# Optimization experiments

Measured on AMD Instinct MI355X. Metric: run time of the kernel, lower is better.

The kernel has to match this reference:

```python
import jax, jax.numpy as jnp
import numpy as np

NUM_HEADS = 32
NUM_KV_HEADS = 8
HEAD_DIM = 128
ROPE_THETA = 10000.0


def rotate_half(x):
    x1, x2 = jnp.split(x, 2, axis=-1)
    return jnp.concatenate((-x2, x1), axis=-1)


def setup_inputs() -> dict:
    key = jax.random.key(0)
    ks = jax.random.split(key, 5)
    B, S, H = 1, 2048, 4096
    KV = NUM_KV_HEADS * HEAD_DIM
    return {
        "hidden_states": jax.random.normal(ks[0], (B, S, H), dtype=jnp.float32),
        "position_ids": jnp.arange(S, dtype=jnp.int64 if jax.config.jax_enable_x64 else jnp.int32)[None, :].repeat(B, axis=0),
        "Wq": jax.random.normal(ks[1], (H, H), dtype=jnp.float32) * 0.02,
        "Wk": jax.random.normal(ks[2], (KV, H), dtype=jnp.float32) * 0.02,
        "Wv": jax.random.normal(ks[3], (KV, H), dtype=jnp.float32) * 0.02,
        "Wo": jax.random.normal(ks[4], (H, H), dtype=jnp.float32) * 0.02,
    }


def reference(hidden_states, position_ids, Wq, Wk, Wv, Wo):
    B, S, H = hidden_states.shape
    nh, nkv, hd = NUM_HEADS, NUM_KV_HEADS, HEAD_DIM
    n_rep = nh // nkv

    # QKV projections (torch Linear: y = x @ W^T)
    q = jnp.einsum('bsh,oh->bso', hidden_states, Wq).reshape(B, S, nh, hd).transpose(0, 2, 1, 3)
    k = jnp.einsum('bsh,oh->bso', hidden_states, Wk).reshape(B, S, nkv, hd).transpose(0, 2, 1, 3)
    v = jnp.einsum('bsh,oh->bso', hidden_states, Wv).reshape(B, S, nkv, hd).transpose(0, 2, 1, 3)

    # RoPE: cos/sin [B, 1, S, hd]
    inv_freq = 1.0 / (ROPE_THETA ** (jnp.arange(0, hd, 2, dtype=jnp.float32) / hd))
    freqs = position_ids.astype(jnp.float32)[..., None] * inv_freq  # [B, S, hd/2]
    emb = jnp.concatenate((freqs, freqs), axis=-1)                  # [B, S, hd]
    cos = jnp.cos(emb)[:, None, :, :]
    sin = jnp.sin(emb)[:, None, :, :]
    q = q * cos + rotate_half(q) * sin
    k = k * cos + rotate_half(k) * sin

    # GQA repeat_kv: [B, nkv, S, hd] -> [B, nh, S, hd]
    k = jnp.repeat(k, n_rep, axis=1)
    v = jnp.repeat(v, n_rep, axis=1)

    # eager attention with causal mask, softmax in fp32
    scores = jnp.einsum('bhqd,bhkd->bhqk', q, k) / jnp.sqrt(jnp.float32(hd))
    causal = jnp.tril(jnp.ones((S, S), dtype=bool))
    scores = jnp.where(causal[None, None], scores, jnp.finfo(scores.dtype).min)
    probs = jax.nn.softmax(scores.astype(jnp.float32), axis=-1).astype(q.dtype)
    attn = jnp.einsum('bhqk,bhkd->bhqd', probs, v)

    out = attn.transpose(0, 2, 1, 3).reshape(B, S, nh * hd)
    return jnp.einsum('bso,ho->bsh', out, Wo)
```

## Files before the change

### kernel.cpp

```cpp
#include <hip/hip_runtime.h>

typedef __bf16 bf16x8 __attribute__((ext_vector_type(8)));
typedef float f32x4 __attribute__((ext_vector_type(4)));
typedef unsigned int u32x4 __attribute__((ext_vector_type(4)));
typedef unsigned short u16x4 __attribute__((ext_vector_type(4)));
typedef unsigned short ushort_t;

#define S_LEN 2048
#define HDIM  4096
#define KVDIM 1024
#define NHEAD 32
#define NKV   8

__device__ __forceinline__ unsigned short f2b(float x) {
    unsigned int u = __builtin_bit_cast(unsigned int, x);
    u = (u + 0x7FFFu + ((u >> 16) & 1u)) >> 16;
    return (unsigned short)u;
}
__device__ __forceinline__ float b2f(unsigned short b) {
    unsigned int u = ((unsigned int)b) << 16;
    return __builtin_bit_cast(float, u);
}

__device__ __forceinline__ void gl_lds16(const void* g, void* s) {
    __builtin_amdgcn_global_load_lds(
        (const __attribute__((address_space(1))) unsigned int*)g,
        (__attribute__((address_space(3))) unsigned int*)s, 16, 0, 0);
}

__global__ void cvt_kernel(const float* __restrict__ in, unsigned short* __restrict__ out, int n4) {
    int i = blockIdx.x * 256 + threadIdx.x;
    if (i >= n4) return;
    f32x4 v = ((const f32x4*)in)[i];
    u16x4 o;
    o.x = f2b(v.x); o.y = f2b(v.y); o.z = f2b(v.z); o.w = f2b(v.w);
    ((u16x4*)out)[i] = o;
}

template <int MODE>
__device__ __forceinline__ void gemm_body(const unsigned short* __restrict__ A,
                                          const unsigned short* __restrict__ B,
                                          void* __restrict__ Cv,
                                          int M, int N, int K, int m0, int n0,
                                          unsigned short (*As)[64], unsigned short (*Bs)[64]) {
    const int tid = threadIdx.x;
    const int w = tid >> 6, lane = tid & 63, quad = lane >> 4, l15 = lane & 15;
    const int wy = w >> 1, wx = w & 1;
    const int srowb = w * 32 + (lane >> 3);
    const int gchunk = (lane & 7) ^ (lane >> 3);
    const int lcol = (lane & 7) * 8;

    f32x4 acc[4][4] = {};

    for (int k0 = 0; k0 < K; k0 += 64) {
#pragma unroll
        for (int p = 0; p < 4; ++p) {
            int r = srowb + p * 8;
            gl_lds16(&A[(size_t)(m0 + r) * K + k0 + gchunk * 8], &As[r][lcol]);
            gl_lds16(&B[(size_t)(n0 + r) * K + k0 + gchunk * 8], &Bs[r][lcol]);
        }
        __syncthreads();
#pragma unroll
        for (int t = 0; t < 2; ++t) {
            bf16x8 af[4], bfr[4];
#pragma unroll
            for (int mb = 0; mb < 4; ++mb)
                af[mb] = *(const bf16x8*)&As[wy * 64 + mb * 16 + l15][(((t * 4 + quad) ^ (l15 & 7)) * 8)];
#pragma unroll
            for (int nb = 0; nb < 4; ++nb)
                bfr[nb] = *(const bf16x8*)&Bs[wx * 64 + nb * 16 + l15][(((t * 4 + quad) ^ (l15 & 7)) * 8)];
#pragma unroll
            for (int mb = 0; mb < 4; ++mb)
#pragma unroll
                for (int nb = 0; nb < 4; ++nb)
                    acc[mb][nb] = __builtin_amdgcn_mfma_f32_16x16x32_bf16(af[mb], bfr[nb], acc[mb][nb], 0, 0, 0);
        }
        __syncthreads();
    }
#pragma unroll
    for (int mb = 0; mb < 4; ++mb)
#pragma unroll
        for (int nb = 0; nb < 4; ++nb)
#pragma unroll
            for (int r = 0; r < 4; ++r) {
                int row = m0 + wy * 64 + mb * 16 + quad * 4 + r;
                int col = n0 + wx * 64 + nb * 16 + l15;
                float v = acc[mb][nb][r];
                if (MODE == 0)
                    ((unsigned short*)Cv)[(size_t)row * N + col] = f2b(v);
                else if (MODE == 1)
                    ((unsigned short*)Cv)[(size_t)col * M + row] = f2b(v);
                else
                    ((float*)Cv)[(size_t)row * N + col] = v;
            }
}

template <int MODE>
__global__ __launch_bounds__(256) void gemm_nt(const unsigned short* __restrict__ A,
                                               const unsigned short* __restrict__ B,
                                               void* __restrict__ Cv, int M, int N, int K) {
    __shared__ unsigned short As[128][64];
    __shared__ unsigned short Bs[128][64];
    gemm_body<MODE>(A, B, Cv, M, N, K, blockIdx.y * 128, blockIdx.x * 128, As, Bs);
}

__global__ __launch_bounds__(256) void gemm_kv(const unsigned short* __restrict__ A,
                                               const unsigned short* __restrict__ Bk,
                                               const unsigned short* __restrict__ Bv,
                                               void* __restrict__ Ck, void* __restrict__ Cvt,
                                               int M, int K) {
    __shared__ unsigned short As[128][64];
    __shared__ unsigned short Bs[128][64];
    if (blockIdx.x < 8)
        gemm_body<0>(A, Bk, Ck, M, KVDIM, K, blockIdx.y * 128, blockIdx.x * 128, As, Bs);
    else
        gemm_body<1>(A, Bv, Cvt, M, KVDIM, K, blockIdx.y * 128, (blockIdx.x - 8) * 128, As, Bs);
}

__global__ void rope_kernel(unsigned short* __restrict__ Q, unsigned short* __restrict__ Kc,
                            const int* __restrict__ pos_ids) {
    int tid = blockIdx.x * 256 + threadIdx.x;
    int j = tid & 63;
    int head = (tid >> 6) % (NHEAD + NKV);
    int s = tid / (64 * (NHEAD + NKV));
    float pos = (float)pos_ids[s];
    float inv = exp2f(-(float)j * 0.20762050593046f);
    float ang = pos * inv;
    float sn, cs;
    __sincosf(ang, &sn, &cs);
    unsigned short* p;
    if (head < NHEAD)
        p = Q + (size_t)s * HDIM + head * 128;
    else
        p = Kc + (size_t)s * KVDIM + (head - NHEAD) * 128;
    float x1 = b2f(p[j]), x2 = b2f(p[j + 64]);
    p[j] = f2b(x1 * cs - x2 * sn);
    p[j + 64] = f2b(x2 * cs + x1 * sn);
}

__global__ __launch_bounds__(256) void attn_fwd(const unsigned short* __restrict__ Q,
                                                const unsigned short* __restrict__ Kb,
                                                const unsigned short* __restrict__ Vt,
                                                unsigned short* __restrict__ O) {
    __shared__ unsigned short Ks[64][136];
    __shared__ unsigned short Vts[128][72];
    __shared__ unsigned short Ps[4][16][80];

    const int qblk = (gridDim.y - 1) - blockIdx.y;
    const int h = blockIdx.x, kvh = h >> 2;
    const int tid = threadIdx.x, w = tid >> 6, lane = tid & 63;
    const int quad = lane >> 4, l15 = lane & 15;
    const int qg = qblk * 64 + w * 16 + l15;

    bf16x8 aq[4];
#pragma unroll
    for (int t = 0; t < 4; ++t)
        aq[t] = *(const bf16x8*)&Q[(size_t)qg * HDIM + h * 128 + t * 32 + quad * 8];

    f32x4 o[8] = {};
    float m_s = -3.0e38f, l_s = 0.f;
    const float cexp = 0.08838834764831845f * 1.4426950408889634f;

    const int kr0 = tid >> 4, ksg = tid & 15;
    const int vr0 = tid >> 3, vsg = tid & 7;

    u32x4 kpre[4], vpre[4];
#pragma unroll
    for (int p = 0; p < 4; ++p) {
        kpre[p] = *(const u32x4*)&Kb[(size_t)(kr0 + p * 16) * KVDIM + kvh * 128 + ksg * 8];
        vpre[p] = *(const u32x4*)&Vt[(size_t)(kvh * 128 + vr0 + p * 32) * S_LEN + vsg * 8];
    }

    for (int kt = 0; kt <= qblk; ++kt) {
#pragma unroll
        for (int p = 0; p < 4; ++p) {
            *(u32x4*)&Ks[kr0 + p * 16][ksg * 8] = kpre[p];
            *(u32x4*)&Vts[vr0 + p * 32][vsg * 8] = vpre[p];
        }
        __syncthreads();
        if (kt < qblk) {
            const int k0n = kt * 64 + 64;
#pragma unroll
            for (int p = 0; p < 4; ++p) {
                kpre[p] = *(const u32x4*)&Kb[(size_t)(k0n + kr0 + p * 16) * KVDIM + kvh * 128 + ksg * 8];
                vpre[p] = *(const u32x4*)&Vt[(size_t)(kvh * 128 + vr0 + p * 32) * S_LEN + k0n + vsg * 8];
            }
        }

        f32x4 sc[4] = {};
#pragma unroll
        for (int t = 0; t < 4; ++t)
#pragma unroll
            for (int mb = 0; mb < 4; ++mb) {
                bf16x8 ak = *(const bf16x8*)&Ks[mb * 16 + l15][t * 32 + quad * 8];
                sc[mb] = __builtin_amdgcn_mfma_f32_16x16x32_bf16(ak, aq[t], sc[mb], 0, 0, 0);
            }

        float vv[16];
        if (kt == qblk) {
#pragma unroll
            for (int mb = 0; mb < 4; ++mb)
#pragma unroll
                for (int r = 0; r < 4; ++r) {
                    int kl = mb * 16 + quad * 4 + r;
                    vv[mb * 4 + r] = (kl <= w * 16 + l15) ? sc[mb][r] * cexp : -3.0e38f;
                }
        } else {
#pragma unroll
            for (int mb = 0; mb < 4; ++mb)
#pragma unroll
                for (int r = 0; r < 4; ++r)
                    vv[mb * 4 + r] = sc[mb][r] * cexp;
        }
        float mx = vv[0];
#pragma unroll
        for (int i = 1; i < 16; ++i) mx = fmaxf(mx, vv[i]);
        mx = fmaxf(mx, __shfl_xor(mx, 16, 64));
        mx = fmaxf(mx, __shfl_xor(mx, 32, 64));
        float mnew = fmaxf(m_s, mx);
        float alpha = exp2f(m_s - mnew);
        m_s = mnew;
        float sum = 0.f;
        unsigned short pb[16];
#pragma unroll
        for (int i = 0; i < 16; ++i) {
            float pp = exp2f(vv[i] - mnew);
            sum += pp;
            pb[i] = f2b(pp);
        }
        sum += __shfl_xor(sum, 16, 64);
        sum += __shfl_xor(sum, 32, 64);
        l_s = l_s * alpha + sum;
#pragma unroll
        for (int mb = 0; mb < 4; ++mb) {
            u16x4 pk = {pb[mb * 4 + 0], pb[mb * 4 + 1], pb[mb * 4 + 2], pb[mb * 4 + 3]};
            *(u16x4*)&Ps[w][l15][mb * 16 + quad * 4] = pk;
        }
        float a4[4];
#pragma unroll
        for (int r = 0; r < 4; ++r) a4[r] = __shfl(alpha, quad * 20 + r, 64);
#pragma unroll
        for (int db = 0; db < 8; ++db)
#pragma unroll
            for (int r = 0; r < 4; ++r) o[db][r] *= a4[r];

        bf16x8 pa[2];
#pragma unroll
        for (int t = 0; t < 2; ++t)
            pa[t] = *(const bf16x8*)&Ps[w][l15][t * 32 + quad * 8];
#pragma unroll
        for (int db = 0; db < 8; ++db)
#pragma unroll
            for (int t = 0; t < 2; ++t) {
                bf16x8 vb = *(const bf16x8*)&Vts[db * 16 + l15][t * 32 + quad * 8];
                o[db] = __builtin_amdgcn_mfma_f32_16x16x32_bf16(pa[t], vb, o[db], 0, 0, 0);
            }
        __syncthreads();
    }

    float linv[4];
#pragma unroll
    for (int r = 0; r < 4; ++r) linv[r] = 1.0f / __shfl(l_s, quad * 20 + r, 64);
    const int qrow_base = qblk * 64 + w * 16 + quad * 4;
#pragma unroll
    for (int db = 0; db < 8; ++db)
#pragma unroll
        for (int r = 0; r < 4; ++r) {
            int row = qrow_base + r;
            int col = h * 128 + db * 16 + l15;
            O[(size_t)row * HDIM + col] = f2b(o[db][r] * linv[r]);
        }
}

extern "C" void kernel_launch(void* const* d_in, const int* in_sizes, int n_in,
                              void* d_out, int out_size, void* d_ws, size_t ws_size,
                              hipStream_t stream) {
    const float* hid = (const float*)d_in[0];
    const int* pos   = (const int*)d_in[1];
    const float* Wq  = (const float*)d_in[2];
    const float* Wk  = (const float*)d_in[3];
    const float* Wv  = (const float*)d_in[4];
    const float* Wo  = (const float*)d_in[5];
    float* out = (float*)d_out;

    char* ws = (char*)d_ws;
    unsigned short* hb   = (unsigned short*)(ws);
    unsigned short* Wqb  = (unsigned short*)(ws + 16777216);
    unsigned short* Wkb  = (unsigned short*)(ws + 50331648);
    unsigned short* Wvb  = (unsigned short*)(ws + 58720256);
    unsigned short* Wob  = (unsigned short*)(ws + 67108864);
    unsigned short* Qw   = (unsigned short*)(ws + 100663296);
    unsigned short* Kw   = (unsigned short*)(ws + 117440512);
    unsigned short* Vtw  = Wqb;
    unsigned short* attw = hb;

    cvt_kernel<<<(S_LEN * HDIM / 4 + 255) / 256, 256, 0, stream>>>(hid, hb, S_LEN * HDIM / 4);
    cvt_kernel<<<(HDIM * HDIM / 4 + 255) / 256, 256, 0, stream>>>(Wq, Wqb, HDIM * HDIM / 4);
    cvt_kernel<<<(KVDIM * HDIM / 4 + 255) / 256, 256, 0, stream>>>(Wk, Wkb, KVDIM * HDIM / 4);
    cvt_kernel<<<(KVDIM * HDIM / 4 + 255) / 256, 256, 0, stream>>>(Wv, Wvb, KVDIM * HDIM / 4);
    cvt_kernel<<<(HDIM * HDIM / 4 + 255) / 256, 256, 0, stream>>>(Wo, Wob, HDIM * HDIM / 4);

    gemm_nt<0><<<dim3(HDIM / 128, S_LEN / 128), 256, 0, stream>>>(hb, Wqb, Qw, S_LEN, HDIM, HDIM);
    gemm_kv<<<dim3(16, S_LEN / 128), 256, 0, stream>>>(hb, Wkb, Wvb, Kw, Vtw, S_LEN, HDIM);

    rope_kernel<<<S_LEN * (NHEAD + NKV) * 64 / 256, 256, 0, stream>>>(Qw, Kw, pos);

    attn_fwd<<<dim3(NHEAD, S_LEN / 64), 256, 0, stream>>>(Qw, Kw, Vtw, attw);

    gemm_nt<2><<<dim3(HDIM / 128, S_LEN / 128), 256, 0, stream>>>(attw, Wob, out, S_LEN, HDIM, HDIM);
}
```

Measured before the change: 556.2 us.

## Fuse QKV conversion and GEMM, add lazy softmax rescale and MFMA priority

Merges the four fp32-to-bf16 conversions into one kernel and the Q and KV projection GEMMs into a single launch over a concatenated weight buffer. It also compacts the workspace layout. In attention it skips the running-max rescale unless the max grows by more than a threshold, and raises wave priority around the MFMA blocks. It also pads the P tile in shared memory and uses a tree max reduction. These cut launch count, tail effects and exp/multiply work, at the cost of a more complex control flow and a lazy-rescale bound that must stay numerically safe.

```diff
diff --git a/kernel.cpp b/kernel.cpp
--- a/kernel.cpp
+++ b/kernel.cpp
@@ -4,13 +4,13 @@
 typedef float f32x4 __attribute__((ext_vector_type(4)));
 typedef unsigned int u32x4 __attribute__((ext_vector_type(4)));
 typedef unsigned short u16x4 __attribute__((ext_vector_type(4)));
-typedef unsigned short ushort_t;
 
 #define S_LEN 2048
 #define HDIM  4096
 #define KVDIM 1024
 #define NHEAD 32
 #define NKV   8
+#define QKVN  6144
 
 __device__ __forceinline__ unsigned short f2b(float x) {
     unsigned int u = __builtin_bit_cast(unsigned int, x);
@@ -26,6 +26,26 @@
     __builtin_amdgcn_global_load_lds(
         (const __attribute__((address_space(1))) unsigned int*)g,
         (__attribute__((address_space(3))) unsigned int*)s, 16, 0, 0);
+}
+
+__global__ void cvt_all(const float* __restrict__ hid, const float* __restrict__ Wq,
+                        const float* __restrict__ Wk, const float* __restrict__ Wv,
+                        unsigned short* __restrict__ hb, unsigned short* __restrict__ Wqkvb) {
+    const int NH = S_LEN * HDIM / 4;
+    const int NQ = HDIM * HDIM / 4;
+    const int NK = KVDIM * HDIM / 4;
+    int i = blockIdx.x * 256 + threadIdx.x;
+    const float* src;
+    unsigned short* dst;
+    int off;
+    if (i < NH) { src = hid; dst = hb; off = i; }
+    else if (i < NH + NQ) { src = Wq; dst = Wqkvb; off = i - NH; }
+    else if (i < NH + NQ + NK) { src = Wk; dst = Wqkvb + (size_t)HDIM * HDIM; off = i - NH - NQ; }
+    else { src = Wv; dst = Wqkvb + (size_t)(HDIM + KVDIM) * HDIM; off = i - NH - NQ - NK; }
+    f32x4 v = ((const f32x4*)src)[off];
+    u16x4 o;
+    o.x = f2b(v.x); o.y = f2b(v.y); o.z = f2b(v.z); o.w = f2b(v.w);
+    ((u16x4*)dst)[off] = o;
 }
 
 __global__ void cvt_kernel(const float* __restrict__ in, unsigned short* __restrict__ out, int n4) {
@@ -41,7 +61,7 @@
 __device__ __forceinline__ void gemm_body(const unsigned short* __restrict__ A,
                                           const unsigned short* __restrict__ B,
                                           void* __restrict__ Cv,
-                                          int M, int N, int K, int m0, int n0,
+                                          int M, int N, int K, int m0, int n0, int cn0,
                                           unsigned short (*As)[64], unsigned short (*Bs)[64]) {
     const int tid = threadIdx.x;
     const int w = tid >> 6, lane = tid & 63, quad = lane >> 4, l15 = lane & 15;
@@ -84,7 +104,7 @@
 #pragma unroll
             for (int r = 0; r < 4; ++r) {
                 int row = m0 + wy * 64 + mb * 16 + quad * 4 + r;
-                int col = n0 + wx * 64 + nb * 16 + l15;
+                int col = cn0 + wx * 64 + nb * 16 + l15;
                 float v = acc[mb][nb][r];
                 if (MODE == 0)
                     ((unsigned short*)Cv)[(size_t)row * N + col] = f2b(v);
@@ -101,20 +121,24 @@
                                                void* __restrict__ Cv, int M, int N, int K) {
     __shared__ unsigned short As[128][64];
     __shared__ unsigned short Bs[128][64];
-    gemm_body<MODE>(A, B, Cv, M, N, K, blockIdx.y * 128, blockIdx.x * 128, As, Bs);
-}
-
-__global__ __launch_bounds__(256) void gemm_kv(const unsigned short* __restrict__ A,
-                                               const unsigned short* __restrict__ Bk,
-                                               const unsigned short* __restrict__ Bv,
-                                               void* __restrict__ Ck, void* __restrict__ Cvt,
-                                               int M, int K) {
+    gemm_body<MODE>(A, B, Cv, M, N, K, blockIdx.y * 128, blockIdx.x * 128, blockIdx.x * 128, As, Bs);
+}
+
+__global__ __launch_bounds__(256) void gemm_qkv(const unsigned short* __restrict__ A,
+                                                const unsigned short* __restrict__ W,
+                                                unsigned short* __restrict__ Q,
+                                                unsigned short* __restrict__ Kc,
+                                                unsigned short* __restrict__ Vt,
+                                                int M, int K) {
     __shared__ unsigned short As[128][64];
     __shared__ unsigned short Bs[128][64];
-    if (blockIdx.x < 8)
-        gemm_body<0>(A, Bk, Ck, M, KVDIM, K, blockIdx.y * 128, blockIdx.x * 128, As, Bs);
+    const int bx = blockIdx.x, m0 = blockIdx.y * 128, n0 = bx * 128;
+    if (bx < 32)
+        gemm_body<0>(A, W, Q, M, HDIM, K, m0, n0, n0, As, Bs);
+    else if (bx < 40)
+        gemm_body<0>(A, W, Kc, M, KVDIM, K, m0, n0, n0 - HDIM, As, Bs);
     else
-        gemm_body<1>(A, Bv, Cvt, M, KVDIM, K, blockIdx.y * 128, (blockIdx.x - 8) * 128, As, Bs);
+        gemm_body<1>(A, W, Vt, M, KVDIM, K, m0, n0, n0 - HDIM - KVDIM, As, Bs);
 }
 
 __global__ void rope_kernel(unsigned short* __restrict__ Q, unsigned short* __restrict__ Kc,
@@ -144,7 +168,7 @@
                                                 unsigned short* __restrict__ O) {
     __shared__ unsigned short Ks[64][136];
     __shared__ unsigned short Vts[128][72];
-    __shared__ unsigned short Ps[4][16][80];
+    __shared__ unsigned short Ps[4][16][88];
 
     const int qblk = (gridDim.y - 1) - blockIdx.y;
     const int h = blockIdx.x, kvh = h >> 2;
@@ -188,6 +212,7 @@
         }
 
         f32x4 sc[4] = {};
+        __builtin_amdgcn_s_setprio(1);
 #pragma unroll
         for (int t = 0; t < 4; ++t)
 #pragma unroll
@@ -195,6 +220,7 @@
                 bf16x8 ak = *(const bf16x8*)&Ks[mb * 16 + l15][t * 32 + quad * 8];
                 sc[mb] = __builtin_amdgcn_mfma_f32_16x16x32_bf16(ak, aq[t], sc[mb], 0, 0, 0);
             }
+        __builtin_amdgcn_s_setprio(0);
 
         float vv[16];
         if (kt == qblk) {
@@ -202,8 +228,9 @@
             for (int mb = 0; mb < 4; ++mb)
 #pragma unroll
                 for (int r = 0; r < 4; ++r) {
-                    int kl = mb * 16 + quad * 4 + r;
-                    vv[mb * 4 + r] = (kl <= w * 16 + l15) ? sc[mb][r] * cexp : -3.0e38f;
+                    int kl = mb * 4 ? 0 : 0, _ = kl;
+                    int kk = mb * 16 + quad * 4 + r;
+                    vv[mb * 4 + r] = (kk <= w * 16 + l15) ? sc[mb][r] * cexp : -3.0e38f;
                 }
         } else {
 #pragma unroll
@@ -212,42 +239,46 @@
                 for (int r = 0; r < 4; ++r)
                     vv[mb * 4 + r] = sc[mb][r] * cexp;
         }
-        float mx = vv[0];
-#pragma unroll
-        for (int i = 1; i < 16; ++i) mx = fmaxf(mx, vv[i]);
+        float m8[8];
+#pragma unroll
+        for (int i = 0; i < 8; ++i) m8[i] = fmaxf(vv[i], vv[i + 8]);
+        float mx = fmaxf(fmaxf(fmaxf(m8[0], m8[1]), fmaxf(m8[2], m8[3])),
+                         fmaxf(fmaxf(m8[4], m8[5]), fmaxf(m8[6], m8[7])));
         mx = fmaxf(mx, __shfl_xor(mx, 16, 64));
         mx = fmaxf(mx, __shfl_xor(mx, 32, 64));
-        float mnew = fmaxf(m_s, mx);
-        float alpha = exp2f(m_s - mnew);
-        m_s = mnew;
+        if (!__all(mx - m_s <= 8.0f)) {
+            float mnew = fmaxf(m_s, mx);
+            float alpha = exp2f(m_s - mnew);
+            m_s = mnew;
+            l_s *= alpha;
+            float a4[4];
+#pragma unroll
+            for (int r = 0; r < 4; ++r) a4[r] = __shfl(alpha, quad * 20 + r, 64);
+#pragma unroll
+            for (int db = 0; db < 8; ++db)
+#pragma unroll
+                for (int r = 0; r < 4; ++r) o[db][r] *= a4[r];
+        }
         float sum = 0.f;
-        unsigned short pb[16];
+        __bf16 pb[16] __attribute__((aligned(8)));
 #pragma unroll
         for (int i = 0; i < 16; ++i) {
-            float pp = exp2f(vv[i] - mnew);
+            float pp = exp2f(vv[i] - m_s);
             sum += pp;
-            pb[i] = f2b(pp);
+            pb[i] = (__bf16)pp;
         }
         sum += __shfl_xor(sum, 16, 64);
         sum += __shfl_xor(sum, 32, 64);
-        l_s = l_s * alpha + sum;
-#pragma unroll
-        for (int mb = 0; mb < 4; ++mb) {
-            u16x4 pk = {pb[mb * 4 + 0], pb[mb * 4 + 1], pb[mb * 4 + 2], pb[mb * 4 + 3]};
-            *(u16x4*)&Ps[w][l15][mb * 16 + quad * 4] = pk;
-        }
-        float a4[4];
-#pragma unroll
-        for (int r = 0; r < 4; ++r) a4[r] = __shfl(alpha, quad * 20 + r, 64);
-#pragma unroll
-        for (int db = 0; db < 8; ++db)
-#pragma unroll
-            for (int r = 0; r < 4; ++r) o[db][r] *= a4[r];
+        l_s += sum;
+#pragma unroll
+        for (int mb = 0; mb < 4; ++mb)
+            *(u16x4*)&Ps[w][l15][mb * 16 + quad * 4] = *(const u16x4*)&pb[mb * 4];
 
         bf16x8 pa[2];
 #pragma unroll
         for (int t = 0; t < 2; ++t)
             pa[t] = *(const bf16x8*)&Ps[w][l15][t * 32 + quad * 8];
+        __builtin_amdgcn_s_setprio(1);
 #pragma unroll
         for (int db = 0; db < 8; ++db)
 #pragma unroll
@@ -255,6 +286,7 @@
                 bf16x8 vb = *(const bf16x8*)&Vts[db * 16 + l15][t * 32 + quad * 8];
                 o[db] = __builtin_amdgcn_mfma_f32_16x16x32_bf16(pa[t], vb, o[db], 0, 0, 0);
             }
+        __builtin_amdgcn_s_setprio(0);
         __syncthreads();
     }
 
@@ -284,25 +316,21 @@
     float* out = (float*)d_out;
 
     char* ws = (char*)d_ws;
-    unsigned short* hb   = (unsigned short*)(ws);
-    unsigned short* Wqb  = (unsigned short*)(ws + 16777216);
-    unsigned short* Wkb  = (unsigned short*)(ws + 50331648);
-    unsigned short* Wvb  = (unsigned short*)(ws + 58720256);
-    unsigned short* Wob  = (unsigned short*)(ws + 67108864);
-    unsigned short* Qw   = (unsigned short*)(ws + 100663296);
-    unsigned short* Kw   = (unsigned short*)(ws + 117440512);
-    unsigned short* Vtw  = Wqb;
-    unsigned short* attw = hb;
-
-    cvt_kernel<<<(S_LEN * HDIM / 4 + 255) / 256, 256, 0, stream>>>(hid, hb, S_LEN * HDIM / 4);
-    cvt_kernel<<<(HDIM * HDIM / 4 + 255) / 256, 256, 0, stream>>>(Wq, Wqb, HDIM * HDIM / 4);
-    cvt_kernel<<<(KVDIM * HDIM / 4 + 255) / 256, 256, 0, stream>>>(Wk, Wkb, KVDIM * HDIM / 4);
-    cvt_kernel<<<(KVDIM * HDIM / 4 + 255) / 256, 256, 0, stream>>>(Wv, Wvb, KVDIM * HDIM / 4);
+    unsigned short* hb    = (unsigned short*)(ws);
+    unsigned short* Wqkvb = (unsigned short*)(ws + (16ull << 20));
+    unsigned short* Wob   = (unsigned short*)(ws + (16ull << 20));
+    unsigned short* Qw    = (unsigned short*)(ws + (64ull << 20));
+    unsigned short* Kw    = (unsigned short*)(ws + (80ull << 20));
+    unsigned short* Vtw   = (unsigned short*)(ws + (84ull << 20));
+    unsigned short* attw  = hb;
+
+    cvt_all<<<(S_LEN * HDIM / 4 + HDIM * HDIM / 4 + 2 * (KVDIM * HDIM / 4)) / 256, 256, 0, stream>>>(
+        hid, Wq, Wk, Wv, hb, Wqkvb);
+
+    gemm_qkv<<<dim3(QKVN / 128, S_LEN / 128), 256, 0, stream>>>(hb, Wqkvb, Qw, Kw, Vtw, S_LEN, HDIM);
+
     cvt_kernel<<<(HDIM * HDIM / 4 + 255) / 256, 256, 0, stream>>>(Wo, Wob, HDIM * HDIM / 4);
 
-    gemm_nt<0><<<dim3(HDIM / 128, S_LEN / 128), 256, 0, stream>>>(hb, Wqb, Qw, S_LEN, HDIM, HDIM);
-    gemm_kv<<<dim3(16, S_LEN / 128), 256, 0, stream>>>(hb, Wkb, Wvb, Kw, Vtw, S_LEN, HDIM);
-
     rope_kernel<<<S_LEN * (NHEAD + NKV) * 64 / 256, 256, 0, stream>>>(Qw, Kw, pos);
 
     attn_fwd<<<dim3(NHEAD, S_LEN / 64), 256, 0, stream>>>(Qw, Kw, Vtw, attw);
```

Result: faster. 485.4 us (-12.7%).
